# Performance work log

Measured on AMD Instinct MI355X. Metric: run time of the kernel, lower is better.

Reference implementation:

```python
import jax, jax.numpy as jnp
import numpy as np

H, D, HID = 16, 128, 2048
B, S = 2, 2048
NUM_BLOCKS, BLOCK_SIZE = 32, 128


def _rope(x, cos, sin):
    # x: [T, H, D]; cos/sin: [T, D/2] (neox / rotate-half style)
    half = x.shape[-1] // 2
    x1, x2 = x[..., :half], x[..., half:]
    c = cos[:, None, :]
    s = sin[:, None, :]
    return jnp.concatenate([x1 * c - x2 * s, x2 * c + x1 * s], axis=-1)


def setup_inputs() -> dict:
    key = jax.random.key(0)
    ks = jax.random.split(key, 6)
    T = B * S
    hidden_states = jax.random.normal(ks[0], (T, HID), jnp.float32)
    wqkv = jax.random.normal(ks[1], (HID, 3 * HID), jnp.float32) * 0.02
    bqkv = jax.random.normal(ks[2], (3 * HID,), jnp.float32) * 0.02
    wo = jax.random.normal(ks[3], (HID, HID), jnp.float32) * 0.02
    # rotary tables, base 10000, dim = head_size
    inv_freq = 1.0 / (10000.0 ** (jnp.arange(0, D, 2, dtype=jnp.float32) / D))  # [D/2]
    pos = jnp.tile(jnp.arange(S, dtype=jnp.float32), B)  # positions per token [T]
    ang = pos[:, None] * inv_freq[None, :]  # [T, D/2]
    cos, sin = jnp.cos(ang), jnp.sin(ang)
    k_cache = jnp.zeros((NUM_BLOCKS, BLOCK_SIZE, H, D), jnp.float32)
    v_cache = jnp.zeros((NUM_BLOCKS, BLOCK_SIZE, H, D), jnp.float32)
    cu_seqlen_prefill = jnp.array([0, S, 2 * S], jnp.int32)
    slots = jnp.arange(T, dtype=jnp.int32)
    return {"hidden_states": hidden_states, "cos": cos, "sin": sin,
            "wqkv": wqkv, "bqkv": bqkv, "wo": wo,
            "k_cache": k_cache, "v_cache": v_cache,
            "cu_seqlen_prefill": cu_seqlen_prefill, "slots": slots, "max_s": S}


def reference(hidden_states, cos, sin, wqkv, bqkv, wo, k_cache, v_cache,
              cu_seqlen_prefill, slots, max_s):
    T = hidden_states.shape[0]
    # fused QKV projection (c_attn)
    qkv = hidden_states @ wqkv + bqkv  # [T, 3*H*D]
    q, k, v = jnp.split(qkv, [H * D, 2 * H * D], axis=1)
    q = q.reshape(T, H, D)
    k = k.reshape(T, H, D)
    v = v.reshape(T, H, D)
    # rotary embedding on q and k (in-place in torch; functional here)
    q = _rope(q, cos, sin)
    k = _rope(k, cos, sin)
    # reshape_and_cache: scatter post-rope k and v into paged KV cache by slot
    kc = k_cache.reshape(-1, H, D).at[slots].set(k).reshape(k_cache.shape)
    vc = v_cache.reshape(-1, H, D).at[slots].set(v).reshape(v_cache.shape)
    # prefill flash attention: varlen causal; equal-length sequences here
    b, s = T // max_s, max_s
    qb = q.reshape(b, s, H, D)
    kb = k.reshape(b, s, H, D)
    vb = v.reshape(b, s, H, D)
    scale = D ** -0.5
    scores = jnp.einsum('bqhd,bkhd->bhqk', qb, kb) * scale  # [B,H,S,S]
    causal = jnp.tril(jnp.ones((s, s), bool))
    scores = jnp.where(causal[None, None], scores, jnp.finfo(scores.dtype).min)
    probs = jax.nn.softmax(scores, axis=-1)
    attn = jnp.einsum('bhqk,bkhd->bqhd', probs, vb).reshape(T, H * D)
    out = attn @ wo  # c_proj, no bias
    return out, kc, vc
```

## Files before the change

kernel.cpp:

```cpp
#include <hip/hip_runtime.h>

using f32x4  = __attribute__((ext_vector_type(4))) float;
using frag16 = __attribute__((ext_vector_type(8))) short;
using s16x4  = __attribute__((ext_vector_type(4))) short;
using s16x8  = __attribute__((ext_vector_type(8))) short;
using u32x4  = __attribute__((ext_vector_type(4))) unsigned;

#define DI __device__ __forceinline__

constexpr int HID  = 2048;
constexpr int NH   = 16;
constexpr int HD   = 128;
constexpr int TT   = 4096;
constexpr int SEQ  = 2048;
constexpr int NQKV = 3 * HID;
constexpr float SCL = 0.08838834764831845f * 1.4426950408889634f;

DI short f2bf(float f) {
  unsigned u = __builtin_bit_cast(unsigned, f);
  unsigned r = (u + 0x7fffu + ((u >> 16) & 1u)) >> 16;
  return (short)r;
}
DI float bf2f(short s) {
  unsigned u = ((unsigned)(unsigned short)s) << 16;
  return __builtin_bit_cast(float, u);
}
DI unsigned cvtpk(float lo, float hi) {
  unsigned r;
  asm("v_cvt_pk_bf16_f32 %0, %1, %2" : "=v"(r) : "v"(lo), "v"(hi));
  return r;
}

struct alignas(8) S4h { short a, b, c, d; };

__global__ void prep(const float* __restrict__ hidden, short* __restrict__ Abf,
                     const float* __restrict__ wqkv, short* __restrict__ Wqkvt,
                     const float* __restrict__ wo, short* __restrict__ Wot) {
  __shared__ float t[64][65];
  const int bid = blockIdx.x;
  const int tid = threadIdx.x;
  if (bid < 8192) {
    int gid = bid * 256 + tid;
    float4 v = ((const float4*)hidden)[gid];
    S4h o{f2bf(v.x), f2bf(v.y), f2bf(v.z), f2bf(v.w)};
    ((S4h*)Abf)[gid] = o;
    return;
  }
  const float* in;
  short* out;
  int ldin, R, bx, by;
  if (bid < 8192 + 3072) {
    int idx = bid - 8192;
    in = wqkv; out = Wqkvt; ldin = NQKV; R = HID;
    bx = idx % 96; by = idx / 96;
  } else {
    int idx = bid - 8192 - 3072;
    in = wo; out = Wot; ldin = HID; R = HID;
    bx = idx % 32; by = idx / 32;
  }
#pragma unroll
  for (int i = 0; i < 4; i++) {
    int idx = i * 256 + tid;
    int r = idx >> 4, c4 = idx & 15;
    size_t gi = (size_t)(by * 64 + r) * ldin + bx * 64 + c4 * 4;
    float4 v = *(const float4*)(in + gi);
    t[r][c4 * 4] = v.x; t[r][c4 * 4 + 1] = v.y;
    t[r][c4 * 4 + 2] = v.z; t[r][c4 * 4 + 3] = v.w;
  }
  __syncthreads();
#pragma unroll
  for (int i = 0; i < 4; i++) {
    int idx = i * 256 + tid;
    int r = idx >> 4, c4 = idx & 15;
    s16x4 o;
#pragma unroll
    for (int j = 0; j < 4; j++) o[j] = f2bf(t[c4 * 4 + j][r]);
    *(s16x4*)(out + (size_t)(bx * 64 + r) * R + by * 64 + c4 * 4) = o;
  }
}

__global__ void post(const short* __restrict__ Kb, const short* __restrict__ Vrow,
                     short* __restrict__ Vt, const int* __restrict__ slots,
                     float* __restrict__ kc, float* __restrict__ vc) {
  __shared__ float t[64][65];
  const int bid = blockIdx.x;
  const int tid = threadIdx.x;
  if (bid < 2048) {
    int bx = bid & 31, by = bid >> 5;
#pragma unroll
    for (int i = 0; i < 4; i++) {
      int idx = i * 256 + tid;
      int r = idx >> 4, c4 = idx & 15;
      size_t gi = (size_t)(by * 64 + r) * HID + bx * 64 + c4 * 4;
      s16x4 v = *(const s16x4*)(Vrow + gi);
#pragma unroll
      for (int j = 0; j < 4; j++) t[r][c4 * 4 + j] = bf2f(v[j]);
    }
    __syncthreads();
#pragma unroll
    for (int i = 0; i < 4; i++) {
      int idx = i * 256 + tid;
      int r = idx >> 4, c4 = idx & 15;
      s16x4 o;
#pragma unroll
      for (int j = 0; j < 4; j++) {
        int c = c4 * 4 + j;
        int cs = (c >> 5) * 32 + ((c >> 2) & 1) * 16 + ((c >> 3) & 3) * 4 + (c & 3);
        o[j] = f2bf(t[cs][r]);
      }
      *(s16x4*)(Vt + (size_t)(bx * 64 + r) * TT + by * 64 + c4 * 4) = o;
    }
    return;
  }
  const int tok = bid - 2048;
  const int slot = slots[tok];
  const short* kr = Kb + (size_t)tok * HID;
  const short* vr = Vrow + (size_t)tok * HID;
  float* kco = kc + (size_t)slot * HID;
  float* vco = vc + (size_t)slot * HID;
  const int i = tid * 8;
  s16x8 k8 = *(const s16x8*)(kr + i);
  s16x8 v8 = *(const s16x8*)(vr + i);
  *(float4*)(kco + i)     = {bf2f(k8[0]), bf2f(k8[1]), bf2f(k8[2]), bf2f(k8[3])};
  *(float4*)(kco + i + 4) = {bf2f(k8[4]), bf2f(k8[5]), bf2f(k8[6]), bf2f(k8[7])};
  *(float4*)(vco + i)     = {bf2f(v8[0]), bf2f(v8[1]), bf2f(v8[2]), bf2f(v8[3])};
  *(float4*)(vco + i + 4) = {bf2f(v8[4]), bf2f(v8[5]), bf2f(v8[6]), bf2f(v8[7])};
}

#define GLDS(src, dst)                                                     \
  __builtin_amdgcn_global_load_lds(                                        \
      (const __attribute__((address_space(1))) void*)(src),                \
      (__attribute__((address_space(3))) void*)(dst), 16, 0, 0)

template <int EPI>
__global__ __launch_bounds__(256, 2) void gemm_bt(
    const short* __restrict__ A, const short* __restrict__ Bt,
    const float* __restrict__ bias, float* __restrict__ Cout,
    const float* __restrict__ cs, const float* __restrict__ sn,
    short* __restrict__ Qb, short* __restrict__ Kb, short* __restrict__ Vrow,
    int M, int N, int K) {
  __shared__ alignas(16) short Al[128 * 64];
  __shared__ alignas(16) short Bl[128 * 64];
  const int tid = threadIdx.x;
  const int wid = tid >> 6, lane = tid & 63;
  const int wr = wid >> 1, wc = wid & 1;
  const int l15 = lane & 15, lg = lane >> 4;
  const int gx = gridDim.x;
  const int id = blockIdx.y * gx + blockIdx.x;
  const int nwg = gx * gridDim.y;
  const int swz = (id & 7) * (nwg >> 3) + (id >> 3);
  const int row0 = (swz / gx) * 128, col0 = (swz % gx) * 128;
  const int lr8 = lane >> 3, l7 = lane & 7;

  f32x4 acc[4][4];
#pragma unroll
  for (int i = 0; i < 4; i++)
#pragma unroll
    for (int j = 0; j < 4; j++) acc[i][j] = {0.f, 0.f, 0.f, 0.f};

  for (int kt = 0; kt < K; kt += 64) {
#pragma unroll
    for (int c = 0; c < 4; c++) {
      int chunk = c * 4 + wid;
      int r = chunk * 8 + lr8;
      int ke = (l7 * 8) ^ ((r & 7) * 8);
      GLDS(A + (size_t)(row0 + r) * K + kt + ke, Al + chunk * 512);
      GLDS(Bt + (size_t)(col0 + r) * K + kt + ke, Bl + chunk * 512);
    }
    __syncthreads();
#pragma unroll
    for (int kk = 0; kk < 2; kk++) {
      frag16 af[4], bfv[4];
#pragma unroll
      for (int ai = 0; ai < 4; ai++) {
        int r = wr * 64 + ai * 16 + l15;
        int k0 = kk * 32 + lg * 8;
        af[ai] = *(const frag16*)(Al + r * 64 + (k0 ^ ((r & 7) * 8)));
      }
#pragma unroll
      for (int bj = 0; bj < 4; bj++) {
        int r = wc * 16 + (bj & 1) * 32 + ((bj >> 1) << 6) + l15;
        int k0 = kk * 32 + lg * 8;
        bfv[bj] = *(const frag16*)(Bl + r * 64 + (k0 ^ ((r & 7) * 8)));
      }
#pragma unroll
      for (int ai = 0; ai < 4; ai++)
#pragma unroll
        for (int bj = 0; bj < 4; bj++)
          acc[ai][bj] = __builtin_amdgcn_mfma_f32_16x16x32_bf16(
              af[ai], bfv[bj], acc[ai][bj], 0, 0, 0);
    }
    __syncthreads();
  }

  if (EPI == 0) {
#pragma unroll
    for (int ai = 0; ai < 4; ai++) {
#pragma unroll
      for (int bj = 0; bj < 4; bj++) {
        int row = row0 + wr * 64 + ai * 16 + lg * 4;
        int col = col0 + wc * 16 + (bj & 1) * 32 + ((bj >> 1) << 6) + l15;
#pragma unroll
        for (int r = 0; r < 4; r++)
          Cout[(size_t)(row + r) * N + col] = acc[ai][bj][r];
      }
    }
  } else {
    const int sec = col0 >> 11;
    const int h = (col0 & 2047) >> 7;
#pragma unroll
    for (int ai = 0; ai < 4; ai++) {
#pragma unroll
      for (int bj = 0; bj < 2; bj++) {
        const int d1 = wc * 16 + bj * 32 + l15;
        const float b1 = bias[col0 + d1];
        const float b2 = bias[col0 + d1 + 64];
        const int base = h * 128 + d1;
#pragma unroll
        for (int r = 0; r < 4; r++) {
          const int tok = row0 + wr * 64 + ai * 16 + lg * 4 + r;
          float v1 = acc[ai][bj][r] + b1;
          float v2 = acc[ai][bj + 2][r] + b2;
          if (sec == 0) {
            float c = cs[tok * 64 + d1], s = sn[tok * 64 + d1];
            Qb[(size_t)tok * HID + base]      = f2bf((v1 * c - v2 * s) * SCL);
            Qb[(size_t)tok * HID + base + 64] = f2bf((v2 * c + v1 * s) * SCL);
          } else if (sec == 1) {
            float c = cs[tok * 64 + d1], s = sn[tok * 64 + d1];
            Kb[(size_t)tok * HID + base]      = f2bf(v1 * c - v2 * s);
            Kb[(size_t)tok * HID + base + 64] = f2bf(v2 * c + v1 * s);
          } else {
            Vrow[(size_t)tok * HID + base]      = f2bf(v1);
            Vrow[(size_t)tok * HID + base + 64] = f2bf(v2);
          }
        }
      }
    }
  }
}

__global__ __launch_bounds__(256, 2) void flash_attn6(
    const short* __restrict__ Qb, const short* __restrict__ Kb,
    const short* __restrict__ Vt, short* __restrict__ attn) {
  __shared__ alignas(16) short Klds[2][64 * 128];
  __shared__ alignas(16) short Vlds[2][128 * 64];

  const int tid = threadIdx.x;
  const int w = tid >> 6, lane = tid & 63;
  const int l15 = lane & 15, lg = lane >> 4;
  const int bid = blockIdx.x;
  const int p = bid >> 5;
  const int bh = bid & 31;
  const int b = bh >> 4, h = bh & 15;

  frag16 ones;
#pragma unroll
  for (int j = 0; j < 8; j++) ones[j] = (short)0x3F80;

  auto stage = [&](int kv0, int buf) {
#pragma unroll
    for (int ci = 0; ci < 4; ci++) {
      int cc = w * 4 + ci;
      int krow = cc * 4 + (lane >> 4);
      int kss = (lane & 15) ^ (krow & 15);
      GLDS(Kb + (size_t)(b * SEQ + kv0 + krow) * HID + h * HD + kss * 8,
           Klds[buf] + cc * 512);
      int vd = cc * 8 + (lane >> 3);
      int vss = (lane & 7) ^ (vd & 7);
      GLDS(Vt + (size_t)(h * HD + vd) * TT + b * SEQ + kv0 + vss * 8,
           Vlds[buf] + cc * 512);
    }
  };

  const int qrowH = (31 - p) * 64 + w * 16;
  const int qrowL = p * 64 + w * 16;
  const int ntH = 32 - p;

  frag16 qfH[4], qfL[4];
  {
    const short* qpH = Qb + (size_t)(b * SEQ + qrowH + l15) * HID + h * HD + lg * 8;
    const short* qpL = Qb + (size_t)(b * SEQ + qrowL + l15) * HID + h * HD + lg * 8;
#pragma unroll
    for (int ds = 0; ds < 4; ds++) {
      qfH[ds] = *(const frag16*)(qpH + ds * 32);
      qfL[ds] = *(const frag16*)(qpL + ds * 32);
    }
  }
  f32x4 oH[8], oL[8];
#pragma unroll
  for (int j = 0; j < 8; j++) { oH[j] = {0.f, 0.f, 0.f, 0.f}; oL[j] = {0.f, 0.f, 0.f, 0.f}; }
  f32x4 laH = {0.f, 0.f, 0.f, 0.f}, laL = {0.f, 0.f, 0.f, 0.f};
  float mrH = -1e30f, mrL = -1e30f;

  auto proc = [&](const frag16 (&qf)[4], f32x4 (&o)[8], f32x4& la, float& mr,
                  bool diag, const short* Kl, const short* Vl) {
    f32x4 sa[4];
#pragma unroll
    for (int f = 0; f < 4; f++) sa[f] = {0.f, 0.f, 0.f, 0.f};
    __builtin_amdgcn_s_setprio(1);
#pragma unroll
    for (int ds = 0; ds < 4; ds++) {
      int phys = (ds * 4 + lg) ^ l15;
#pragma unroll
      for (int f = 0; f < 4; f++) {
        frag16 kf = *(const frag16*)(Kl + (f * 16 + l15) * 128 + phys * 8);
        sa[f] = __builtin_amdgcn_mfma_f32_16x16x32_bf16(kf, qf[ds], sa[f], 0, 0, 0);
      }
    }
    __builtin_amdgcn_s_setprio(0);
    if (diag) {
      int ql = 16 * w + l15;
#pragma unroll
      for (int f = 0; f < 4; f++)
#pragma unroll
        for (int r = 0; r < 4; r++)
          if (f * 16 + lg * 4 + r > ql) sa[f][r] = -1e30f;
    }
    float pm = sa[0][0];
#pragma unroll
    for (int f = 0; f < 4; f++)
#pragma unroll
      for (int r = 0; r < 4; r++) pm = fmaxf(pm, sa[f][r]);
    pm = fmaxf(pm, __shfl_xor(pm, 16));
    pm = fmaxf(pm, __shfl_xor(pm, 32));
    if (__any(pm > mr + 8.f)) {
      float mn = fmaxf(mr, pm);
      float frl = exp2f(mr - mn);
      mr = mn;
      float fr4[4];
#pragma unroll
      for (int r = 0; r < 4; r++)
        fr4[r] = __shfl(frl, lg * 16 + lg * 4 + r);
#pragma unroll
      for (int r = 0; r < 4; r++) {
        la[r] *= fr4[r];
#pragma unroll
        for (int j = 0; j < 8; j++) o[j][r] *= fr4[r];
      }
    }
    float pe[4][4];
#pragma unroll
    for (int f = 0; f < 4; f++)
#pragma unroll
      for (int r = 0; r < 4; r++) pe[f][r] = exp2f(sa[f][r] - mr);
    u32x4 w0, w1;
    w0[0] = cvtpk(pe[0][0], pe[0][1]); w0[1] = cvtpk(pe[0][2], pe[0][3]);
    w0[2] = cvtpk(pe[1][0], pe[1][1]); w0[3] = cvtpk(pe[1][2], pe[1][3]);
    w1[0] = cvtpk(pe[2][0], pe[2][1]); w1[1] = cvtpk(pe[2][2], pe[2][3]);
    w1[2] = cvtpk(pe[3][0], pe[3][1]); w1[3] = cvtpk(pe[3][2], pe[3][3]);
    frag16 pf0 = __builtin_bit_cast(frag16, w0);
    frag16 pf1 = __builtin_bit_cast(frag16, w1);
    __builtin_amdgcn_s_setprio(1);
    la = __builtin_amdgcn_mfma_f32_16x16x32_bf16(pf0, ones, la, 0, 0, 0);
    la = __builtin_amdgcn_mfma_f32_16x16x32_bf16(pf1, ones, la, 0, 0, 0);
#pragma unroll
    for (int j = 0; j < 8; j++) {
      int d = j * 16 + l15;
      int p0 = lg ^ (d & 7);
      int p1 = (4 + lg) ^ (d & 7);
      frag16 vf0 = *(const frag16*)(Vl + d * 64 + p0 * 8);
      frag16 vf1 = *(const frag16*)(Vl + d * 64 + p1 * 8);
      o[j] = __builtin_amdgcn_mfma_f32_16x16x32_bf16(pf0, vf0, o[j], 0, 0, 0);
      o[j] = __builtin_amdgcn_mfma_f32_16x16x32_bf16(pf1, vf1, o[j], 0, 0, 0);
    }
    __builtin_amdgcn_s_setprio(0);
  };

  stage(0, 0);
  __syncthreads();

  int cur = 0;
  for (int t = 0; t < ntH; t++) {
    if (t + 1 < ntH) stage((t + 1) * 64, cur ^ 1);
    const short* Kl = &Klds[cur][0];
    const short* Vl = &Vlds[cur][0];
    proc(qfH, oH, laH, mrH, t == ntH - 1, Kl, Vl);
    if (t <= p) proc(qfL, oL, laL, mrL, t == p, Kl, Vl);
    __syncthreads();
    cur ^= 1;
  }

  {
    float inv[4];
#pragma unroll
    for (int r = 0; r < 4; r++) inv[r] = 1.f / laH[r];
    short* op = attn + (size_t)(b * SEQ + qrowH + lg * 4) * HID + h * HD + l15;
#pragma unroll
    for (int j = 0; j < 8; j++)
#pragma unroll
      for (int r = 0; r < 4; r++)
        op[(size_t)r * HID + j * 16] = f2bf(oH[j][r] * inv[r]);
  }
  {
    float inv[4];
#pragma unroll
    for (int r = 0; r < 4; r++) inv[r] = 1.f / laL[r];
    short* op = attn + (size_t)(b * SEQ + qrowL + lg * 4) * HID + h * HD + l15;
#pragma unroll
    for (int j = 0; j < 8; j++)
#pragma unroll
      for (int r = 0; r < 4; r++)
        op[(size_t)r * HID + j * 16] = f2bf(oL[j][r] * inv[r]);
  }
}

extern "C" void kernel_launch(void* const* d_in, const int* in_sizes, int n_in,
                              void* d_out, int out_size, void* d_ws, size_t ws_size,
                              hipStream_t stream) {
  const float* hidden = (const float*)d_in[0];
  const float* cosb   = (const float*)d_in[1];
  const float* sinb   = (const float*)d_in[2];
  const float* wqkv   = (const float*)d_in[3];
  const float* bqkv   = (const float*)d_in[4];
  const float* wo     = (const float*)d_in[5];
  const int*   slots  = (const int*)d_in[9];

  float* out = (float*)d_out;
  float* kc  = out + (size_t)TT * HID;
  float* vc  = kc + (size_t)TT * HID;

  short* ws    = (short*)d_ws;
  short* Abf   = ws;
  short* Wqkvt = Abf + 8388608;
  short* Wot   = Wqkvt + 12582912;
  short* Qb    = Wot + 4194304;
  short* Kb    = Qb + 8388608;
  short* Vrow  = Kb + 8388608;
  short* Vt    = Vrow + 8388608;
  short* attnb = Abf;

  prep<<<8192 + 3072 + 1024, 256, 0, stream>>>(hidden, Abf, wqkv, Wqkvt, wo, Wot);
  gemm_bt<1><<<dim3(48, 32), 256, 0, stream>>>(
      Abf, Wqkvt, bqkv, nullptr, cosb, sinb, Qb, Kb, Vrow, TT, NQKV, HID);
  post<<<2048 + 4096, 256, 0, stream>>>(Kb, Vrow, Vt, slots, kc, vc);
  flash_attn6<<<512, 256, 0, stream>>>(Qb, Kb, Vt, attnb);
  gemm_bt<0><<<dim3(16, 32), 256, 0, stream>>>(
      attnb, Wot, nullptr, out, nullptr, nullptr, nullptr, nullptr, nullptr,
      TT, HID, HID);
}
```

Measured before the change: 283.5 us.

## Rewrite flash attention with one Q tile per block and 32-wide KV tiles

Replaces the paired high/low query-tile flash attention kernel, which balanced causal work, with a simpler kernel where each block handles a single 64-row Q tile. Each step streams 32-row K/V tiles, which halves LDS use and halves the accumulator registers. Launch bounds rise to 4 blocks per CU and the grid doubles to 1024 blocks, heavy blocks first. This trades the built-in causal load balancing for higher occupancy and more blocks. It also adds more barriers per KV row, and some waves skip compute on diagonal tiles while still taking part in staging.

```diff
diff --git a/kernel.cpp b/kernel.cpp
--- a/kernel.cpp
+++ b/kernel.cpp
@@ -239,169 +239,139 @@
   }
 }
 
-__global__ __launch_bounds__(256, 2) void flash_attn6(
+__global__ __launch_bounds__(256, 4) void flash_attn10(
     const short* __restrict__ Qb, const short* __restrict__ Kb,
     const short* __restrict__ Vt, short* __restrict__ attn) {
-  __shared__ alignas(16) short Klds[2][64 * 128];
-  __shared__ alignas(16) short Vlds[2][128 * 64];
+  __shared__ alignas(16) short Klds[2][32 * 128];
+  __shared__ alignas(16) short Vlds[2][128 * 32];
 
   const int tid = threadIdx.x;
   const int w = tid >> 6, lane = tid & 63;
   const int l15 = lane & 15, lg = lane >> 4;
   const int bid = blockIdx.x;
-  const int p = bid >> 5;
+  const int s = 31 - (bid >> 5);
   const int bh = bid & 31;
   const int b = bh >> 4, h = bh & 15;
 
   frag16 ones;
 #pragma unroll
-  for (int j = 0; j < 8; j++) ones[j] = (short)0x3F80;
+  for (int q = 0; q < 8; q++) ones[q] = (short)0x3F80;
 
   auto stage = [&](int kv0, int buf) {
 #pragma unroll
-    for (int ci = 0; ci < 4; ci++) {
-      int cc = w * 4 + ci;
-      int krow = cc * 4 + (lane >> 4);
-      int kss = (lane & 15) ^ (krow & 15);
+    for (int ci = 0; ci < 2; ci++) {
+      int e = ci * 256 + w * 64 + lane;
+      int krow = e >> 4;
+      int kss = (e & 15) ^ (krow & 15);
       GLDS(Kb + (size_t)(b * SEQ + kv0 + krow) * HID + h * HD + kss * 8,
-           Klds[buf] + cc * 512);
-      int vd = cc * 8 + (lane >> 3);
-      int vss = (lane & 7) ^ (vd & 7);
+           Klds[buf] + (ci * 256 + w * 64) * 8);
+      int vd = e >> 2;
+      int vss = (e & 3) ^ (vd & 3);
       GLDS(Vt + (size_t)(h * HD + vd) * TT + b * SEQ + kv0 + vss * 8,
-           Vlds[buf] + cc * 512);
+           Vlds[buf] + (ci * 256 + w * 64) * 8);
     }
   };
 
-  const int qrowH = (31 - p) * 64 + w * 16;
-  const int qrowL = p * 64 + w * 16;
-  const int ntH = 32 - p;
-
-  frag16 qfH[4], qfL[4];
+  const int qrow0 = s * 64 + w * 16;
+  const int nt = 2 * s + 2;
+
+  frag16 qf[4];
   {
-    const short* qpH = Qb + (size_t)(b * SEQ + qrowH + l15) * HID + h * HD + lg * 8;
-    const short* qpL = Qb + (size_t)(b * SEQ + qrowL + l15) * HID + h * HD + lg * 8;
-#pragma unroll
-    for (int ds = 0; ds < 4; ds++) {
-      qfH[ds] = *(const frag16*)(qpH + ds * 32);
-      qfL[ds] = *(const frag16*)(qpL + ds * 32);
-    }
-  }
-  f32x4 oH[8], oL[8];
-#pragma unroll
-  for (int j = 0; j < 8; j++) { oH[j] = {0.f, 0.f, 0.f, 0.f}; oL[j] = {0.f, 0.f, 0.f, 0.f}; }
-  f32x4 laH = {0.f, 0.f, 0.f, 0.f}, laL = {0.f, 0.f, 0.f, 0.f};
-  float mrH = -1e30f, mrL = -1e30f;
-
-  auto proc = [&](const frag16 (&qf)[4], f32x4 (&o)[8], f32x4& la, float& mr,
-                  bool diag, const short* Kl, const short* Vl) {
-    f32x4 sa[4];
-#pragma unroll
-    for (int f = 0; f < 4; f++) sa[f] = {0.f, 0.f, 0.f, 0.f};
-    __builtin_amdgcn_s_setprio(1);
-#pragma unroll
-    for (int ds = 0; ds < 4; ds++) {
-      int phys = (ds * 4 + lg) ^ l15;
-#pragma unroll
-      for (int f = 0; f < 4; f++) {
-        frag16 kf = *(const frag16*)(Kl + (f * 16 + l15) * 128 + phys * 8);
-        sa[f] = __builtin_amdgcn_mfma_f32_16x16x32_bf16(kf, qf[ds], sa[f], 0, 0, 0);
-      }
-    }
-    __builtin_amdgcn_s_setprio(0);
-    if (diag) {
-      int ql = 16 * w + l15;
-#pragma unroll
-      for (int f = 0; f < 4; f++)
-#pragma unroll
-        for (int r = 0; r < 4; r++)
-          if (f * 16 + lg * 4 + r > ql) sa[f][r] = -1e30f;
-    }
-    float pm = sa[0][0];
-#pragma unroll
-    for (int f = 0; f < 4; f++)
-#pragma unroll
-      for (int r = 0; r < 4; r++) pm = fmaxf(pm, sa[f][r]);
-    pm = fmaxf(pm, __shfl_xor(pm, 16));
-    pm = fmaxf(pm, __shfl_xor(pm, 32));
-    if (__any(pm > mr + 8.f)) {
-      float mn = fmaxf(mr, pm);
-      float frl = exp2f(mr - mn);
-      mr = mn;
-      float fr4[4];
-#pragma unroll
-      for (int r = 0; r < 4; r++)
-        fr4[r] = __shfl(frl, lg * 16 + lg * 4 + r);
-#pragma unroll
-      for (int r = 0; r < 4; r++) {
-        la[r] *= fr4[r];
-#pragma unroll
-        for (int j = 0; j < 8; j++) o[j][r] *= fr4[r];
-      }
-    }
-    float pe[4][4];
-#pragma unroll
-    for (int f = 0; f < 4; f++)
-#pragma unroll
-      for (int r = 0; r < 4; r++) pe[f][r] = exp2f(sa[f][r] - mr);
-    u32x4 w0, w1;
-    w0[0] = cvtpk(pe[0][0], pe[0][1]); w0[1] = cvtpk(pe[0][2], pe[0][3]);
-    w0[2] = cvtpk(pe[1][0], pe[1][1]); w0[3] = cvtpk(pe[1][2], pe[1][3]);
-    w1[0] = cvtpk(pe[2][0], pe[2][1]); w1[1] = cvtpk(pe[2][2], pe[2][3]);
-    w1[2] = cvtpk(pe[3][0], pe[3][1]); w1[3] = cvtpk(pe[3][2], pe[3][3]);
-    frag16 pf0 = __builtin_bit_cast(frag16, w0);
-    frag16 pf1 = __builtin_bit_cast(frag16, w1);
-    __builtin_amdgcn_s_setprio(1);
-    la = __builtin_amdgcn_mfma_f32_16x16x32_bf16(pf0, ones, la, 0, 0, 0);
-    la = __builtin_amdgcn_mfma_f32_16x16x32_bf16(pf1, ones, la, 0, 0, 0);
-#pragma unroll
-    for (int j = 0; j < 8; j++) {
-      int d = j * 16 + l15;
-      int p0 = lg ^ (d & 7);
-      int p1 = (4 + lg) ^ (d & 7);
-      frag16 vf0 = *(const frag16*)(Vl + d * 64 + p0 * 8);
-      frag16 vf1 = *(const frag16*)(Vl + d * 64 + p1 * 8);
-      o[j] = __builtin_amdgcn_mfma_f32_16x16x32_bf16(pf0, vf0, o[j], 0, 0, 0);
-      o[j] = __builtin_amdgcn_mfma_f32_16x16x32_bf16(pf1, vf1, o[j], 0, 0, 0);
-    }
-    __builtin_amdgcn_s_setprio(0);
-  };
+    const short* qp = Qb + (size_t)(b * SEQ + qrow0 + l15) * HID + h * HD + lg * 8;
+#pragma unroll
+    for (int ds = 0; ds < 4; ds++) qf[ds] = *(const frag16*)(qp + ds * 32);
+  }
+  f32x4 o[8];
+#pragma unroll
+  for (int q = 0; q < 8; q++) o[q] = {0.f, 0.f, 0.f, 0.f};
+  f32x4 la = {0.f, 0.f, 0.f, 0.f};
+  float mr = -1e30f;
 
   stage(0, 0);
   __syncthreads();
 
   int cur = 0;
-  for (int t = 0; t < ntH; t++) {
-    if (t + 1 < ntH) stage((t + 1) * 64, cur ^ 1);
-    const short* Kl = &Klds[cur][0];
-    const short* Vl = &Vlds[cur][0];
-    proc(qfH, oH, laH, mrH, t == ntH - 1, Kl, Vl);
-    if (t <= p) proc(qfL, oL, laL, mrL, t == p, Kl, Vl);
+  for (int t = 0; t < nt; t++) {
+    const int kv0 = t * 32;
+    if (t + 1 < nt) stage(kv0 + 32, cur ^ 1);
+    if (kv0 <= qrow0 + 15) {
+      const short* Kl = &Klds[cur][0];
+      const short* Vl = &Vlds[cur][0];
+      f32x4 sa[2];
+      sa[0] = {0.f, 0.f, 0.f, 0.f};
+      sa[1] = {0.f, 0.f, 0.f, 0.f};
+      __builtin_amdgcn_s_setprio(1);
+#pragma unroll
+      for (int ds = 0; ds < 4; ds++) {
+        int phys = (ds * 4 + lg) ^ l15;
+#pragma unroll
+        for (int f = 0; f < 2; f++) {
+          frag16 kf = *(const frag16*)(Kl + (f * 16 + l15) * 128 + phys * 8);
+          sa[f] = __builtin_amdgcn_mfma_f32_16x16x32_bf16(kf, qf[ds], sa[f], 0, 0, 0);
+        }
+      }
+      __builtin_amdgcn_s_setprio(0);
+      if (kv0 + 31 > qrow0) {
+        int ql = qrow0 + l15 - kv0;
+#pragma unroll
+        for (int f = 0; f < 2; f++)
+#pragma unroll
+          for (int r = 0; r < 4; r++)
+            if (f * 16 + lg * 4 + r > ql) sa[f][r] = -1e30f;
+      }
+      float pm = fmaxf(
+          fmaxf(fmaxf(sa[0][0], sa[0][1]), fmaxf(sa[0][2], sa[0][3])),
+          fmaxf(fmaxf(sa[1][0], sa[1][1]), fmaxf(sa[1][2], sa[1][3])));
+      pm = fmaxf(pm, __shfl_xor(pm, 16));
+      pm = fmaxf(pm, __shfl_xor(pm, 32));
+      if (__any(pm > mr + 8.f)) {
+        float mn = fmaxf(mr, pm);
+        float frl = exp2f(mr - mn);
+        mr = mn;
+        float fr4[4];
+#pragma unroll
+        for (int r = 0; r < 4; r++)
+          fr4[r] = __shfl(frl, lg * 16 + lg * 4 + r);
+#pragma unroll
+        for (int r = 0; r < 4; r++) {
+          la[r] *= fr4[r];
+#pragma unroll
+          for (int q = 0; q < 8; q++) o[q][r] *= fr4[r];
+        }
+      }
+      float pe[2][4];
+#pragma unroll
+      for (int f = 0; f < 2; f++)
+#pragma unroll
+        for (int r = 0; r < 4; r++) pe[f][r] = exp2f(sa[f][r] - mr);
+      u32x4 w0;
+      w0[0] = cvtpk(pe[0][0], pe[0][1]); w0[1] = cvtpk(pe[0][2], pe[0][3]);
+      w0[2] = cvtpk(pe[1][0], pe[1][1]); w0[3] = cvtpk(pe[1][2], pe[1][3]);
+      frag16 pf0 = __builtin_bit_cast(frag16, w0);
+      __builtin_amdgcn_s_setprio(1);
+      la = __builtin_amdgcn_mfma_f32_16x16x32_bf16(pf0, ones, la, 0, 0, 0);
+#pragma unroll
+      for (int q = 0; q < 8; q++) {
+        int d = q * 16 + l15;
+        int phys = lg ^ (d & 3);
+        frag16 vf = *(const frag16*)(Vl + d * 32 + phys * 8);
+        o[q] = __builtin_amdgcn_mfma_f32_16x16x32_bf16(pf0, vf, o[q], 0, 0, 0);
+      }
+      __builtin_amdgcn_s_setprio(0);
+    }
     __syncthreads();
     cur ^= 1;
   }
 
-  {
-    float inv[4];
-#pragma unroll
-    for (int r = 0; r < 4; r++) inv[r] = 1.f / laH[r];
-    short* op = attn + (size_t)(b * SEQ + qrowH + lg * 4) * HID + h * HD + l15;
-#pragma unroll
-    for (int j = 0; j < 8; j++)
-#pragma unroll
-      for (int r = 0; r < 4; r++)
-        op[(size_t)r * HID + j * 16] = f2bf(oH[j][r] * inv[r]);
-  }
-  {
-    float inv[4];
-#pragma unroll
-    for (int r = 0; r < 4; r++) inv[r] = 1.f / laL[r];
-    short* op = attn + (size_t)(b * SEQ + qrowL + lg * 4) * HID + h * HD + l15;
-#pragma unroll
-    for (int j = 0; j < 8; j++)
-#pragma unroll
-      for (int r = 0; r < 4; r++)
-        op[(size_t)r * HID + j * 16] = f2bf(oL[j][r] * inv[r]);
-  }
+  float inv[4];
+#pragma unroll
+  for (int r = 0; r < 4; r++) inv[r] = 1.f / la[r];
+  short* op = attn + (size_t)(b * SEQ + qrow0 + lg * 4) * HID + h * HD + l15;
+#pragma unroll
+  for (int q = 0; q < 8; q++)
+#pragma unroll
+    for (int r = 0; r < 4; r++)
+      op[(size_t)r * HID + q * 16] = f2bf(o[q][r] * inv[r]);
 }
 
 extern "C" void kernel_launch(void* const* d_in, const int* in_sizes, int n_in,
@@ -433,7 +403,7 @@
   gemm_bt<1><<<dim3(48, 32), 256, 0, stream>>>(
       Abf, Wqkvt, bqkv, nullptr, cosb, sinb, Qb, Kb, Vrow, TT, NQKV, HID);
   post<<<2048 + 4096, 256, 0, stream>>>(Kb, Vrow, Vt, slots, kc, vc);
-  flash_attn6<<<512, 256, 0, stream>>>(Qb, Kb, Vt, attnb);
+  flash_attn10<<<1024, 256, 0, stream>>>(Qb, Kb, Vt, attnb);
   gemm_bt<0><<<dim3(16, 32), 256, 0, stream>>>(
       attnb, Wot, nullptr, out, nullptr, nullptr, nullptr, nullptr, nullptr,
       TT, HID, HID);
```

Result: slower. 300.7 us (+6.1%).
